# Kernel tuning notes

Hardware: AMD Instinct MI355X
Metric: run time of the kernel (lower is better)

## Reference

```python
import jax, jax.numpy as jnp
from jax import lax
import numpy as np

MAX_ITERS = 20  # module hardcodes self.max_iters = 20


def setup_inputs() -> dict:
    key = jax.random.key(0)
    k1, k2 = jax.random.split(key)
    B, H, W, C, K = 16, 96, 96, 256, 21
    x = jax.random.normal(k1, (B, H, W, C), dtype=jnp.float32)
    N = H * W
    init_idx = jax.random.randint(k2, (B, K), 0, N, dtype=jnp.int64)
    return {"x": x, "init_idx": init_idx}


def _kmeans(x_flat, init_idx):
    # x_flat: [B, N, C]; init_idx: [B, K]
    B, N, C = x_flat.shape
    K = init_idx.shape[1]
    # initial centroids: gather K points per batch
    cent0 = jnp.take_along_axis(x_flat, init_idx[..., None], axis=1)  # [B, K, C]
    x_sq = jnp.sum(x_flat * x_flat, axis=-1, keepdims=True)  # [B, N, 1] (constant term)

    def step(cent, _):
        d = x_sq - 2.0 * jnp.einsum('bnc,bkc->bnk', x_flat, cent) \
            + jnp.sum(cent * cent, axis=-1)[:, None, :]  # [B, N, K]
        assign = jnp.argmin(d, axis=-1)  # [B, N]
        onehot = jax.nn.one_hot(assign, K, dtype=x_flat.dtype)  # [B, N, K]
        sums = jnp.einsum('bnk,bnc->bkc', onehot, x_flat)  # scatter-add
        counts = jnp.sum(onehot, axis=1)  # [B, K]
        # scatter-mean; keep previous centroid for empty clusters
        new_cent = jnp.where(counts[..., None] > 0,
                             sums / jnp.maximum(counts, 1.0)[..., None],
                             cent)
        return new_cent, None

    cent, _ = lax.scan(step, cent0, None, length=MAX_ITERS)
    return cent  # [B, K, C]


def reference(x, init_idx):
    B, H, W, C = x.shape
    x_flat = x.reshape(B, H * W, C)
    return _kmeans(x_flat, init_idx)
```

## Files before the change

### kernel.cpp

```cpp
#include <hip/hip_runtime.h>


#define BB 16
#define NN 9216
#define CC 256
#define KK 21
#define ITERS 20
#define QTR 2304

__device__ __forceinline__ float mul_sep(float a, float b) {
  float t = a * b;
  asm("" : "+v"(t));
  return t;
}

__device__ float np_half_sq(const float* v) {
  float r[8];
  #pragma unroll
  for (int j = 0; j < 8; ++j) r[j] = mul_sep(v[j], v[j]);
  for (int i = 8; i < 128; i += 8) {
    #pragma unroll
    for (int j = 0; j < 8; ++j) r[j] = __fadd_rn(r[j], mul_sep(v[i + j], v[i + j]));
  }
  return __fadd_rn(__fadd_rn(__fadd_rn(r[0], r[1]), __fadd_rn(r[2], r[3])),
                   __fadd_rn(__fadd_rn(r[4], r[5]), __fadd_rn(r[6], r[7])));
}

__global__ __launch_bounds__(512) void decode_idx(
    const void* __restrict__ raw, int* __restrict__ out) {
  __shared__ int all_ok;
  if (threadIdx.x == 0) all_ok = 1;
  __syncthreads();
  const long long* p64 = (const long long*)raw;
  const int* p32 = (const int*)raw;
  int t = threadIdx.x;
  long long v64 = 0;
  if (t < BB * KK) {
    v64 = p64[t];
    if (v64 < 0 || v64 >= NN) atomicAnd(&all_ok, 0);
  }
  __syncthreads();
  if (t < BB * KK) out[t] = all_ok ? (int)v64 : p32[t];
}

__global__ __launch_bounds__(256) void gather_init(
    const float* __restrict__ x, const int* __restrict__ idx_dec,
    float* __restrict__ cent, float* __restrict__ csq) {
  __shared__ float row[CC];
  int bk = blockIdx.x;
  int b = bk / KK;
  int c = threadIdx.x;
  int idx = idx_dec[bk];
  float v = x[((size_t)b * NN + idx) * CC + c];
  cent[(size_t)bk * CC + c] = v;
  row[c] = v;
  __syncthreads();
  if (threadIdx.x == 0)
    csq[bk] = __fadd_rn(np_half_sq(row), np_half_sq(row + 128));
}

__global__ __launch_bounds__(256) void assign_np(
    const float* __restrict__ x, const float* __restrict__ cent,
    const float* __restrict__ csq, int* __restrict__ assign) {
  const int nb = NN / 256;
  int b = blockIdx.x / nb;
  int n = (blockIdx.x % nb) * 256 + threadIdx.x;
  const float* xp = x + ((size_t)b * NN + n) * CC;
  const float* cp = cent + (size_t)b * KK * CC;
  const float* cq = csq + b * KK;

  float q[KK][4];
  #pragma unroll
  for (int k = 0; k < KK; ++k)
    #pragma unroll
    for (int j = 0; j < 4; ++j) q[k][j] = 0.f;
  float rA[8], rB[8];
  #pragma unroll
  for (int j = 0; j < 8; ++j) { rA[j] = 0.f; rB[j] = 0.f; }

#define CHUNK16(C0, R)                                                        \
  do {                                                                        \
    float xv[16];                                                             \
    {                                                                         \
      float4 t0 = *(const float4*)(xp + (C0));                                \
      float4 t1 = *(const float4*)(xp + (C0) + 4);                            \
      float4 t2 = *(const float4*)(xp + (C0) + 8);                            \
      float4 t3 = *(const float4*)(xp + (C0) + 12);                           \
      xv[0] = t0.x; xv[1] = t0.y; xv[2] = t0.z; xv[3] = t0.w;                 \
      xv[4] = t1.x; xv[5] = t1.y; xv[6] = t1.z; xv[7] = t1.w;                 \
      xv[8] = t2.x; xv[9] = t2.y; xv[10] = t2.z; xv[11] = t2.w;               \
      xv[12] = t3.x; xv[13] = t3.y; xv[14] = t3.z; xv[15] = t3.w;             \
    }                                                                         \
    _Pragma("unroll")                                                         \
    for (int g = 0; g < 16; g += 8) {                                         \
      _Pragma("unroll")                                                       \
      for (int j = 0; j < 8; ++j)                                             \
        R[j] = __fadd_rn(R[j], mul_sep(xv[g + j], xv[g + j]));                \
    }                                                                         \
    _Pragma("unroll")                                                         \
    for (int k = 0; k < KK; ++k) {                                            \
      const float* cpk = cp + k * CC + (C0);        \
      _Pragma("unroll")                                                       \
      for (int g2 = 0; g2 < 16; g2 += 4) {                                    \
        _Pragma("unroll")                                                     \
        for (int j = 0; j < 4; ++j)                                           \
          q[k][j] = __fadd_rn(q[k][j], mul_sep(xv[g2 + j], cpk[g2 + j]));     \
      }                                                                       \
    }                                                                         \
  } while (0)

  for (int c0 = 0; c0 < 128; c0 += 16) CHUNK16(c0, rA);
  for (int c0 = 128; c0 < 256; c0 += 16) CHUNK16(c0, rB);
#undef CHUNK16

  float hA = __fadd_rn(__fadd_rn(__fadd_rn(rA[0], rA[1]), __fadd_rn(rA[2], rA[3])),
                       __fadd_rn(__fadd_rn(rA[4], rA[5]), __fadd_rn(rA[6], rA[7])));
  float hB = __fadd_rn(__fadd_rn(__fadd_rn(rB[0], rB[1]), __fadd_rn(rB[2], rB[3])),
                       __fadd_rn(__fadd_rn(rB[4], rB[5]), __fadd_rn(rB[6], rB[7])));
  float xsq = __fadd_rn(hA, hB);

  float best = INFINITY;
  int bestk = 0;
  #pragma unroll
  for (int k = 0; k < KK; ++k) {
    float dk = __fadd_rn(__fadd_rn(q[k][0], q[k][2]), __fadd_rn(q[k][1], q[k][3]));
    float d = __fadd_rn(__fsub_rn(xsq, __fmul_rn(2.0f, dk)), cq[k]);
    if (d < best) { best = d; bestk = k; }
  }
  assign[(size_t)b * NN + n] = bestk;
}

__global__ __launch_bounds__(256) void update_np(
    const float* __restrict__ x, const int* __restrict__ assign,
    float* __restrict__ cent, float* __restrict__ csq) {
  __shared__ int idx_lds[4][QTR];
  __shared__ int wcnt[4];
  __shared__ float row[CC];
  int bk = blockIdx.x;
  int b = bk / KK, k = bk % KK;
  int c = threadIdx.x;
  int lane = threadIdx.x & 63, w = threadIdx.x >> 6;

  const int* ap = assign + (size_t)b * NN + w * QTR;
  int cnt = 0;
  for (int i = 0; i < QTR; i += 64) {
    int a = ap[i + lane];
    unsigned long long m = __ballot(a == k);
    if (a == k) {
      int pos = cnt + (int)__popcll(m & ((1ull << lane) - 1ull));
      idx_lds[w][pos] = w * QTR + i + lane;
    }
    cnt += (int)__popcll(m);
  }
  if (lane == 0) wcnt[w] = cnt;
  __syncthreads();

  const float* xb = x + (size_t)b * NN * CC + c;
  float s = 0.f;
  int total = 0;
  #pragma unroll 1
  for (int ww = 0; ww < 4; ++ww) {
    int cw = wcnt[ww];
    total += cw;
    const int* lst = idx_lds[ww];
    int i = 0;
    for (; i + 8 <= cw; i += 8) {
      float v[8];
      #pragma unroll
      for (int j = 0; j < 8; ++j) v[j] = xb[(size_t)lst[i + j] * CC];
      #pragma unroll
      for (int j = 0; j < 8; ++j) s = __fadd_rn(s, v[j]);
    }
    for (; i < cw; ++i) s = __fadd_rn(s, xb[(size_t)lst[i] * CC]);
  }

  float old = cent[(size_t)bk * CC + c];
  float dv = s / fmaxf((float)total, 1.0f);
  float nc = (total > 0) ? dv : old;
  cent[(size_t)bk * CC + c] = nc;
  row[c] = nc;
  __syncthreads();
  if (threadIdx.x == 0)
    csq[bk] = __fadd_rn(np_half_sq(row), np_half_sq(row + 128));
}

extern "C" void kernel_launch(void* const* d_in, const int* in_sizes, int n_in,
                              void* d_out, int out_size, void* d_ws, size_t ws_size,
                              hipStream_t stream) {
  const float* x = (const float*)d_in[0];
  float* cent = (float*)d_out;

  char* ws = (char*)d_ws;
  int* assign = (int*)ws;
  float* csq = (float*)(ws + (size_t)BB * NN * 4);
  int* idx_dec = (int*)(csq + BB * KK);

  decode_idx<<<1, 512, 0, stream>>>(d_in[1], idx_dec);
  gather_init<<<BB * KK, 256, 0, stream>>>(x, idx_dec, cent, csq);
  for (int it = 0; it < ITERS; ++it) {
    assign_np<<<BB * (NN / 256), 256, 0, stream>>>(x, cent, csq, assign);
    update_np<<<BB * KK, 256, 0, stream>>>(x, assign, cent, csq);
  }
}
```

Baseline: 3.526 ms.

## Split centroid update into compaction, channel-split gather, and norm kernels

After: 3.839 ms. +8.9%, slower.

```diff
diff --git a/kernel.cpp b/kernel.cpp
--- a/kernel.cpp
+++ b/kernel.cpp
@@ -130,15 +130,13 @@
   assign[(size_t)b * NN + n] = bestk;
 }
 
-__global__ __launch_bounds__(256) void update_np(
-    const float* __restrict__ x, const int* __restrict__ assign,
-    float* __restrict__ cent, float* __restrict__ csq) {
+__global__ __launch_bounds__(256) void compact_np(
+    const int* __restrict__ assign, int* __restrict__ lists,
+    int* __restrict__ counts) {
   __shared__ int idx_lds[4][QTR];
   __shared__ int wcnt[4];
-  __shared__ float row[CC];
   int bk = blockIdx.x;
   int b = bk / KK, k = bk % KK;
-  int c = threadIdx.x;
   int lane = threadIdx.x & 63, w = threadIdx.x >> 6;
 
   const int* ap = assign + (size_t)b * NN + w * QTR;
@@ -155,30 +153,64 @@
   if (lane == 0) wcnt[w] = cnt;
   __syncthreads();
 
+  int base = 0;
+  #pragma unroll
+  for (int ww = 0; ww < 4; ++ww) if (ww < w) base += wcnt[ww];
+  int* gl = lists + (size_t)bk * NN;
+  for (int i = lane; i < cnt; i += 64) gl[base + i] = idx_lds[w][i];
+  if (threadIdx.x == 0)
+    counts[bk] = wcnt[0] + wcnt[1] + wcnt[2] + wcnt[3];
+}
+
+__global__ __launch_bounds__(64) void update_gather(
+    const float* __restrict__ x, const int* __restrict__ lists,
+    const int* __restrict__ counts, float* __restrict__ cent) {
+  int blk = blockIdx.x;
+  int bk = blk >> 2, g = blk & 3;
+  int b = bk / KK;
+  int c = g * 64 + threadIdx.x;
+  int total = counts[bk];
+  const int* lst = lists + (size_t)bk * NN;
   const float* xb = x + (size_t)b * NN * CC + c;
+
   float s = 0.f;
-  int total = 0;
-  #pragma unroll 1
-  for (int ww = 0; ww < 4; ++ww) {
-    int cw = wcnt[ww];
-    total += cw;
-    const int* lst = idx_lds[ww];
+  if (total > 0) {
     int i = 0;
-    for (; i + 8 <= cw; i += 8) {
-      float v[8];
-      #pragma unroll
-      for (int j = 0; j < 8; ++j) v[j] = xb[(size_t)lst[i + j] * CC];
-      #pragma unroll
-      for (int j = 0; j < 8; ++j) s = __fadd_rn(s, v[j]);
+    for (; i + 16 <= total; i += 16) {
+      int nn[16];
+      float v[16];
+      #pragma unroll
+      for (int j = 0; j < 16; ++j) nn[j] = lst[i + j];
+      #pragma unroll
+      for (int j = 0; j < 16; ++j) v[j] = xb[(size_t)nn[j] * CC];
+      #pragma unroll
+      for (int j = 0; j < 16; ++j) s = __fadd_rn(s, v[j]);
     }
-    for (; i < cw; ++i) s = __fadd_rn(s, xb[(size_t)lst[i] * CC]);
+    if (i < total) {
+      int rem = total - i;
+      int nn[16];
+      float v[16];
+      #pragma unroll
+      for (int j = 0; j < 16; ++j) nn[j] = lst[(j < rem) ? (i + j) : i];
+      #pragma unroll
+      for (int j = 0; j < 16; ++j) v[j] = xb[(size_t)nn[j] * CC];
+      #pragma unroll
+      for (int j = 0; j < 16; ++j)
+        if (j < rem) s = __fadd_rn(s, v[j]);
+    }
   }
 
   float old = cent[(size_t)bk * CC + c];
   float dv = s / fmaxf((float)total, 1.0f);
   float nc = (total > 0) ? dv : old;
   cent[(size_t)bk * CC + c] = nc;
-  row[c] = nc;
+}
+
+__global__ __launch_bounds__(256) void csq_np(
+    const float* __restrict__ cent, float* __restrict__ csq) {
+  __shared__ float row[CC];
+  int bk = blockIdx.x;
+  row[threadIdx.x] = cent[(size_t)bk * CC + threadIdx.x];
   __syncthreads();
   if (threadIdx.x == 0)
     csq[bk] = __fadd_rn(np_half_sq(row), np_half_sq(row + 128));
@@ -191,14 +223,18 @@
   float* cent = (float*)d_out;
 
   char* ws = (char*)d_ws;
-  int* assign = (int*)ws;
-  float* csq = (float*)(ws + (size_t)BB * NN * 4);
+  int* lists = (int*)ws;
+  int* assign = lists + (size_t)BB * KK * NN;
+  int* counts = assign + (size_t)BB * NN;
+  float* csq = (float*)(counts + BB * KK);
   int* idx_dec = (int*)(csq + BB * KK);
 
   decode_idx<<<1, 512, 0, stream>>>(d_in[1], idx_dec);
   gather_init<<<BB * KK, 256, 0, stream>>>(x, idx_dec, cent, csq);
   for (int it = 0; it < ITERS; ++it) {
     assign_np<<<BB * (NN / 256), 256, 0, stream>>>(x, cent, csq, assign);
-    update_np<<<BB * KK, 256, 0, stream>>>(x, assign, cent, csq);
-  }
-}
+    compact_np<<<BB * KK, 256, 0, stream>>>(assign, lists, counts);
+    update_gather<<<BB * KK * 4, 64, 0, stream>>>(x, lists, counts, cent);
+    csq_np<<<BB * KK, 256, 0, stream>>>(cent, csq);
+  }
+}
```
